# Kernel tuning notes

Hardware: AMD Instinct MI355X
Metric: run time of the kernel (lower is better)

## Reference

```python
import jax, jax.numpy as jnp
import numpy as np

V = 30      # vocab
D = 512     # hidden


def gru_cell(x, h, W_ih, W_hh, b_ih, b_hh):
    # PyTorch GRU cell math. x: [B, in], h: [B, D]
    gi = x @ W_ih.T + b_ih          # [B, 3D]
    gh = h @ W_hh.T + b_hh          # [B, 3D]
    i_r, i_z, i_n = jnp.split(gi, 3, axis=-1)
    h_r, h_z, h_n = jnp.split(gh, 3, axis=-1)
    r = jax.nn.sigmoid(i_r + h_r)
    z = jax.nn.sigmoid(i_z + h_z)
    n = jnp.tanh(i_n + r * h_n)
    return (1.0 - z) * n + z * h


def setup_inputs() -> dict:
    key = jax.random.key(0)
    ks = jax.random.split(key, 16)
    B, T, S = 64, 200, 1024
    p = 0.05  # param scale
    return {
        "initial_decoder_hidden": jax.random.normal(ks[0], (2, B, D), jnp.float32),
        "targets": jax.random.randint(ks[1], (B, T), 0, V),
        "encoder_outputs": jax.random.normal(ks[2], (B, S, D), jnp.float32),
        "W_ih0": jax.random.normal(ks[3], (3 * D, V), jnp.float32) * p,
        "W_hh0": jax.random.normal(ks[4], (3 * D, D), jnp.float32) * p,
        "b_ih0": jax.random.normal(ks[5], (3 * D,), jnp.float32) * p,
        "b_hh0": jax.random.normal(ks[6], (3 * D,), jnp.float32) * p,
        "W_ih1": jax.random.normal(ks[7], (3 * D, D), jnp.float32) * p,
        "W_hh1": jax.random.normal(ks[8], (3 * D, D), jnp.float32) * p,
        "b_ih1": jax.random.normal(ks[9], (3 * D,), jnp.float32) * p,
        "b_hh1": jax.random.normal(ks[10], (3 * D,), jnp.float32) * p,
        "W_out": jax.random.normal(ks[11], (D, 2 * D), jnp.float32) * p,
        "W_tok": jax.random.normal(ks[12], (V, D), jnp.float32) * p,
        "b_tok": jax.random.normal(ks[13], (V,), jnp.float32) * p,
    }


def reference(initial_decoder_hidden, targets, encoder_outputs,
              W_ih0, W_hh0, b_ih0, b_hh0,
              W_ih1, W_hh1, b_ih1, b_hh1,
              W_out, W_tok, b_tok):
    # Teacher-forced decode. Original feeds one_hot(targets[:,0]) at t=0,
    # then one_hot(targets[:,t]) AFTER step t, i.e. step t>0 consumes
    # one_hot(targets[:, t-1]).
    B, T = targets.shape
    idx = jnp.concatenate([targets[:, :1], targets[:, :-1]], axis=1)  # [B, T]
    xs = jax.nn.one_hot(idx, V, dtype=jnp.float32)                    # [B, T, V]
    xs = jnp.swapaxes(xs, 0, 1)                                       # [T, B, V]

    mem = encoder_outputs  # [B, S, D]

    def step(carry, x):
        h0, h1 = carry
        h0 = gru_cell(x, h0, W_ih0, W_hh0, b_ih0, b_hh0)
        h1 = gru_cell(h0, h1, W_ih1, W_hh1, b_ih1, b_hh1)
        q = h1                                              # [B, D] top-layer hidden
        scores = jnp.einsum("bd,bsd->bs", q, mem)           # dot attention
        a = jax.nn.softmax(scores, axis=-1)                 # [B, S]
        c = jnp.einsum("bs,bsd->bd", a, mem)                # context [B, D]
        attn_h = jnp.tanh(jnp.concatenate([c, q], axis=-1) @ W_out.T)  # [B, D]
        logits = attn_h @ W_tok.T + b_tok                   # [B, V]
        return (h0, h1), logits

    h_init = (initial_decoder_hidden[0], initial_decoder_hidden[1])
    _, logits = jax.lax.scan(step, h_init, xs)              # [T, B, V]
    return jnp.swapaxes(logits, 0, 1)                       # [B, T, V]
```

## Files before the change

kernel.cpp:

```cpp
#include <hip/hip_runtime.h>

#define TT 200
#define SS 1024
#define DD 512
#define VV 30
#define BB 64
#define BBDD (BB*DD)

#define WS_H0   0
#define WS_GI   (2*BBDD)
#define WS_H1A  (WS_GI + 2*1536*64)
#define WS_CALL (WS_H1A + 200*BBDD)

typedef __attribute__((ext_vector_type(4))) float f4;

__device__ __forceinline__ float dot4(f4 a, f4 b) {
  return a.x*b.x + a.y*b.y + a.z*b.z + a.w*b.w;
}
__device__ __forceinline__ float sigmoidf_(float x) { return 1.f/(1.f + __expf(-x)); }

__device__ __forceinline__ void gl_lds16(const void* g, void* l) {
  __builtin_amdgcn_global_load_lds(
      (const __attribute__((address_space(1))) unsigned int*)g,
      (__attribute__((address_space(3))) unsigned int*)l,
      16, 0, 0);
}

__device__ __forceinline__ void stage64(const float* src, float* TILE, int wv, int lane) {
  #pragma unroll
  for (int rr = 0; rr < 8; ++rr) {
    const int row = wv*8 + rr;
    const float* g = src + (size_t)row*DD + lane*4;
    gl_lds16(g,       TILE + row*516);
    gl_lds16(g + 256, TILE + row*516 + 256);
  }
}

__device__ __forceinline__ void wave_dots(const float* TILE, const float* W, const float* bias,
                                          float* GH, int w_id, int wv, int lane) {
  const int c0 = wv*3, c1 = c0+1, c2 = c0+2;
  const int R0 = __builtin_amdgcn_readfirstlane(((c0>>3)<<9) + w_id*8 + (c0&7));
  const int R1 = __builtin_amdgcn_readfirstlane(((c1>>3)<<9) + w_id*8 + (c1&7));
  const int R2 = __builtin_amdgcn_readfirstlane(((c2>>3)<<9) + w_id*8 + (c2&7));
  const f4* w0 = (const f4*)(W + (size_t)R0*DD);
  const f4* w1 = (const f4*)(W + (size_t)R1*DD);
  const f4* w2 = (const f4*)(W + (size_t)R2*DD);
  const f4* hv4 = (const f4*)TILE + (size_t)lane*129;
  float a0=0.f, a1=0.f, a2=0.f;
  #pragma unroll 4
  for (int kq = 0; kq < 128; ++kq) {
    f4 h = hv4[kq];
    a0 += dot4(h, w0[kq]); a1 += dot4(h, w1[kq]); a2 += dot4(h, w2[kq]);
  }
  GH[c0*64 + lane] = a0 + bias[R0];
  GH[c1*64 + lane] = a1 + bias[R1];
  GH[c2*64 + lane] = a2 + bias[R2];
}

__device__ __forceinline__ void wave_dots_g(const float* TILE, const float* W, const float* bias,
                                            float* gi, int w_id, int wv, int lane) {
  const int c0 = wv*3, c1 = c0+1, c2 = c0+2;
  const int R0 = __builtin_amdgcn_readfirstlane(((c0>>3)<<9) + w_id*8 + (c0&7));
  const int R1 = __builtin_amdgcn_readfirstlane(((c1>>3)<<9) + w_id*8 + (c1&7));
  const int R2 = __builtin_amdgcn_readfirstlane(((c2>>3)<<9) + w_id*8 + (c2&7));
  const f4* w0 = (const f4*)(W + (size_t)R0*DD);
  const f4* w1 = (const f4*)(W + (size_t)R1*DD);
  const f4* w2 = (const f4*)(W + (size_t)R2*DD);
  const f4* hv4 = (const f4*)TILE + (size_t)lane*129;
  float a0=0.f, a1=0.f, a2=0.f;
  #pragma unroll 4
  for (int kq = 0; kq < 128; ++kq) {
    f4 h = hv4[kq];
    a0 += dot4(h, w0[kq]); a1 += dot4(h, w1[kq]); a2 += dot4(h, w2[kq]);
  }
  gi[(size_t)R0*64 + lane] = a0 + bias[R0];
  gi[(size_t)R1*64 + lane] = a1 + bias[R1];
  gi[(size_t)R2*64 + lane] = a2 + bias[R2];
}

__launch_bounds__(512, 1)
__global__ void k_gru0(const float* __restrict__ h0prev, const int* __restrict__ targets,
                       const float* __restrict__ W_ih0, const float* __restrict__ W_hh0,
                       const float* __restrict__ b_ih0, const float* __restrict__ b_hh0,
                       float* __restrict__ h0out, int tokcol) {
  __shared__ float SM[34560];
  float* const TILE = SM;
  float* const GHX  = SM + 33024;
  const int tid = threadIdx.x, bid = blockIdx.x;
  const int lane = tid & 63, wv = tid >> 6;
  stage64(h0prev, TILE, wv, lane);
  __syncthreads();
  wave_dots(TILE, W_hh0, b_hh0, GHX, bid, wv, lane);
  __syncthreads();
  const int dl = tid >> 6, bb = tid & 63, d = bid*8 + dl;
  const int tok = targets[bb*TT + tokcol];
  float gir = W_ih0[(size_t)d*VV + tok]          + b_ih0[d];
  float giz = W_ih0[(size_t)(DD + d)*VV + tok]   + b_ih0[DD + d];
  float gin = W_ih0[(size_t)(2*DD + d)*VV + tok] + b_ih0[2*DD + d];
  float r_ = sigmoidf_(gir + GHX[(0*8 + dl)*64 + bb]);
  float z_ = sigmoidf_(giz + GHX[(1*8 + dl)*64 + bb]);
  float n_ = tanhf(gin + r_*GHX[(2*8 + dl)*64 + bb]);
  float h0old = TILE[bb*516 + d];
  h0out[(size_t)bb*DD + d] = (1.f - z_)*n_ + z_*h0old;
}

__launch_bounds__(512, 1)
__global__ void k_pro1(const float* __restrict__ h0buf0, const int* __restrict__ targets,
                       const float* __restrict__ W_ih0, const float* __restrict__ W_hh0,
                       const float* __restrict__ b_ih0, const float* __restrict__ b_hh0,
                       const float* __restrict__ W_ih1, const float* __restrict__ b_ih1,
                       float* __restrict__ h0buf1, float* __restrict__ gibuf0) {
  __shared__ float SM[34560];
  float* const TILE = SM;
  float* const GHX  = SM + 33024;
  const int tid = threadIdx.x, bid = blockIdx.x;
  const int lane = tid & 63, wv = tid >> 6;
  stage64(h0buf0, TILE, wv, lane);
  __syncthreads();
  if (bid < 64) {
    wave_dots(TILE, W_hh0, b_hh0, GHX, bid, wv, lane);
    __syncthreads();
    const int dl = tid >> 6, bb = tid & 63, d = bid*8 + dl;
    const int tok = targets[bb*TT + 0];
    float gir = W_ih0[(size_t)d*VV + tok]          + b_ih0[d];
    float giz = W_ih0[(size_t)(DD + d)*VV + tok]   + b_ih0[DD + d];
    float gin = W_ih0[(size_t)(2*DD + d)*VV + tok] + b_ih0[2*DD + d];
    float r_ = sigmoidf_(gir + GHX[(0*8 + dl)*64 + bb]);
    float z_ = sigmoidf_(giz + GHX[(1*8 + dl)*64 + bb]);
    float n_ = tanhf(gin + r_*GHX[(2*8 + dl)*64 + bb]);
    float h0old = TILE[bb*516 + d];
    h0buf1[(size_t)bb*DD + d] = (1.f - z_)*n_ + z_*h0old;
  } else {
    wave_dots_g(TILE, W_ih1, b_ih1, gibuf0, bid - 64, wv, lane);
  }
}

__launch_bounds__(512, 1)
__global__ void k_chain(const float* __restrict__ h0rd, float* __restrict__ h0wr,
                        const float* __restrict__ h1src, float* __restrict__ h1dst,
                        const float* __restrict__ gird, float* __restrict__ giwr,
                        const int* __restrict__ targets,
                        const float* __restrict__ W_ih0, const float* __restrict__ W_hh0,
                        const float* __restrict__ b_ih0, const float* __restrict__ b_hh0,
                        const float* __restrict__ W_hh1, const float* __restrict__ b_hh1,
                        const float* __restrict__ W_ih1, const float* __restrict__ b_ih1,
                        int t) {
  __shared__ float SM[34560];
  float* const TILE = SM;
  float* const GHX  = SM + 33024;
  const int tid = threadIdx.x, bid = blockIdx.x;
  const int lane = tid & 63, wv = tid >> 6;
  const int dl = tid >> 6, bb = tid & 63;

  if (bid < 64) {
    if (t <= 197) {
      const int d = bid*8 + dl;
      stage64(h0rd, TILE, wv, lane);
      __syncthreads();
      wave_dots(TILE, W_hh0, b_hh0, GHX, bid, wv, lane);
      __syncthreads();
      const int tok = targets[bb*TT + (t + 1)];
      float gir = W_ih0[(size_t)d*VV + tok]          + b_ih0[d];
      float giz = W_ih0[(size_t)(DD + d)*VV + tok]   + b_ih0[DD + d];
      float gin = W_ih0[(size_t)(2*DD + d)*VV + tok] + b_ih0[2*DD + d];
      float r_ = sigmoidf_(gir + GHX[(0*8 + dl)*64 + bb]);
      float z_ = sigmoidf_(giz + GHX[(1*8 + dl)*64 + bb]);
      float n_ = tanhf(gin + r_*GHX[(2*8 + dl)*64 + bb]);
      float h0old = TILE[bb*516 + d];
      h0wr[(size_t)bb*DD + d] = (1.f - z_)*n_ + z_*h0old;
    }
  } else if (bid < 128) {
    const int w_id = bid - 64;
    const int d = w_id*8 + dl;
    stage64(h1src, TILE, wv, lane);
    __syncthreads();
    wave_dots(TILE, W_hh1, b_hh1, GHX, w_id, wv, lane);
    float h1old = TILE[bb*516 + d];
    __syncthreads();
    float gir = gird[(size_t)(0*DD + d)*64 + bb];
    float giz = gird[(size_t)(1*DD + d)*64 + bb];
    float gin = gird[(size_t)(2*DD + d)*64 + bb];
    float r_ = sigmoidf_(gir + GHX[(0*8 + dl)*64 + bb]);
    float z_ = sigmoidf_(giz + GHX[(1*8 + dl)*64 + bb]);
    float n_ = tanhf(gin + r_*GHX[(2*8 + dl)*64 + bb]);
    h1dst[(size_t)bb*DD + d] = (1.f - z_)*n_ + z_*h1old;
  } else {
    if (t <= 198) {
      stage64(h0rd, TILE, wv, lane);
      __syncthreads();
      wave_dots_g(TILE, W_ih1, b_ih1, giwr, bid - 128, wv, lane);
    }
  }
}

__launch_bounds__(512, 1)
__global__ void k_attn_all(const float* __restrict__ h1a, const float* __restrict__ mem,
                           float* __restrict__ call) {
  __shared__ float SM[37792];
  float* const QL  = SM + 16512;
  float* const SCR = SM + 37152;
  const int tid = threadIdx.x, bid = blockIdx.x;
  const int lane = tid & 63, wv = tid >> 6;
  const int b = bid / 5, tt = bid % 5;
  const int g = lane >> 2, sub = lane & 3;

  #pragma unroll
  for (int rr = 0; rr < 5; ++rr) {
    const int row = wv*5 + rr;
    const float* src = h1a + ((size_t)(tt*40 + row)*BB + b)*DD + lane*4;
    gl_lds16(src,       QL + row*516);
    gl_lds16(src + 256, QL + row*516 + 256);
  }
  const float* msrc = mem + (size_t)b*SS*DD;
  #pragma unroll
  for (int rr = 0; rr < 2; ++rr) {
    const int row = wv*2 + rr;
    const float* gsp = msrc + (size_t)row*DD + lane*4;
    gl_lds16(gsp,       SM + row*516);
    gl_lds16(gsp + 256, SM + row*516 + 256);
  }
  __syncthreads();

  f4 aa[5], ab[5]; float m[5], l[5];
  #pragma unroll
  for (int r = 0; r < 5; ++r) { aa[r] = (f4)0.f; ab[r] = (f4)0.f; m[r] = -3e38f; l[r] = 0.f; }

  int buf = 0;
  for (int tl = 0; tl < 64; ++tl) {
    if (tl + 1 < 64) {
      float* nb = SM + (buf^1)*8256;
      #pragma unroll
      for (int rr = 0; rr < 2; ++rr) {
        const int row = wv*2 + rr;
        const float* gsp = msrc + (size_t)(tl+1)*16*DD + (size_t)row*DD + lane*4;
        gl_lds16(gsp,       nb + row*516);
        gl_lds16(gsp + 256, nb + row*516 + 256);
      }
    }
    const f4* mtf4 = (const f4*)(SM + buf*8256);
    const f4* qlf4 = (const f4*)QL;

    float p[5] = {0.f, 0.f, 0.f, 0.f, 0.f};
    #pragma unroll 4
    for (int k = 0; k < 32; ++k) {
      const int idx = sub*32 + ((k + sub) & 31);
      const f4 mv = mtf4[g*129 + idx];
      #pragma unroll
      for (int r = 0; r < 5; ++r)
        p[r] += dot4(mv, qlf4[(wv*5 + r)*129 + idx]);
    }
    #pragma unroll
    for (int r = 0; r < 5; ++r) {
      p[r] += __shfl_xor(p[r], 1);
      p[r] += __shfl_xor(p[r], 2);
    }
    if (sub == 0) {
      #pragma unroll
      for (int r = 0; r < 5; ++r) SCR[wv*80 + r*16 + g] = p[r];
    }

    #pragma unroll
    for (int r = 0; r < 5; ++r) {
      float mx = SCR[wv*80 + r*16];
      #pragma unroll
      for (int s = 1; s < 16; ++s) mx = fmaxf(mx, SCR[wv*80 + r*16 + s]);
      const float mnew = fmaxf(m[r], mx);
      const float esc = __expf(m[r] - mnew);
      aa[r] *= esc; ab[r] *= esc; l[r] *= esc;
      m[r] = mnew;
    }
    for (int s = 0; s < 16; ++s) {
      const f4 ma = mtf4[s*129 + lane];
      const f4 mb = mtf4[s*129 + lane + 64];
      #pragma unroll
      for (int r = 0; r < 5; ++r) {
        const float w = __expf(SCR[wv*80 + r*16 + s] - m[r]);
        aa[r] += w*ma; ab[r] += w*mb; l[r] += w;
      }
    }
    __syncthreads();
    buf ^= 1;
  }

  #pragma unroll
  for (int r = 0; r < 5; ++r) {
    const float inv = 1.f / l[r];
    float* dst = call + ((size_t)(tt*40 + wv*5 + r)*BB + b)*DD;
    *(f4*)(dst + lane*4)       = aa[r]*inv;
    *(f4*)(dst + lane*4 + 256) = ab[r]*inv;
  }
}

__launch_bounds__(512, 1)
__global__ void k_outproj(const float* __restrict__ call, const float* __restrict__ h1a,
                          const float* __restrict__ W_out, const float* __restrict__ W_tok,
                          const float* __restrict__ b_tok, float* __restrict__ out) {
  __shared__ float SM[4352 + 33024];
  float* const XR = SM;
  float* const AH = SM + 4352;
  const int tid = threadIdx.x, bid = blockIdx.x;
  const int lane = tid & 63, wv = tid >> 6;
  const int rowbase = bid * 64;

  float acc[8][8];
  #pragma unroll
  for (int r = 0; r < 8; ++r)
    #pragma unroll
    for (int j = 0; j < 8; ++j) acc[r][j] = 0.f;

  for (int kc = 0; kc < 16; ++kc) {
    __syncthreads();
    {
      const int row = tid >> 3;
      const int kp  = (tid & 7) * 8;
      const int k   = kc*64 + kp;
      const size_t grow = (size_t)(rowbase + row) * DD;
      const float* src = (k < DD) ? (call + grow + k) : (h1a + grow + (k - DD));
      f4 v0 = *(const f4*)src;
      f4 v1 = *(const f4*)(src + 4);
      *(f4*)&XR[row*68 + kp]     = v0;
      *(f4*)&XR[row*68 + kp + 4] = v1;
    }
    __syncthreads();
    for (int k4 = 0; k4 < 16; ++k4) {
      f4 w4[8];
      #pragma unroll
      for (int j = 0; j < 8; ++j)
        w4[j] = *(const f4*)&W_out[(size_t)(lane*8 + j)*(2*DD) + kc*64 + k4*4];
      #pragma unroll
      for (int r = 0; r < 8; ++r) {
        const f4 x4 = *(const f4*)&XR[(wv*8 + r)*68 + k4*4];
        #pragma unroll
        for (int j = 0; j < 8; ++j) acc[r][j] += dot4(x4, w4[j]);
      }
    }
  }
  #pragma unroll
  for (int r = 0; r < 8; ++r) {
    f4 t0, t1;
    t0.x = tanhf(acc[r][0]); t0.y = tanhf(acc[r][1]); t0.z = tanhf(acc[r][2]); t0.w = tanhf(acc[r][3]);
    t1.x = tanhf(acc[r][4]); t1.y = tanhf(acc[r][5]); t1.z = tanhf(acc[r][6]); t1.w = tanhf(acc[r][7]);
    *(f4*)&AH[(wv*8 + r)*516 + lane*8]     = t0;
    *(f4*)&AH[(wv*8 + r)*516 + lane*8 + 4] = t1;
  }
  __syncthreads();
  const int v = tid & 31;
  const int rq = tid >> 5;
  if (v < VV) {
    for (int it = 0; it < 4; ++it) {
      const int row = rq + it*16;
      float s = 0.f;
      const f4* ar = (const f4*)&AH[row*516];
      const f4* wt = (const f4*)&W_tok[(size_t)v*DD];
      #pragma unroll 4
      for (int k4 = 0; k4 < 128; ++k4) s += dot4(ar[k4], wt[k4]);
      const int gr = rowbase + row;
      const int t = gr >> 6, b = gr & 63;
      out[((size_t)b*TT + t)*VV + v] = s + b_tok[v];
    }
  }
}

extern "C" void kernel_launch(void* const* d_in, const int* in_sizes, int n_in,
                              void* d_out, int out_size, void* d_ws, size_t ws_size,
                              hipStream_t stream) {
  const float* h_init = (const float*)d_in[0];
  const int*   targets= (const int*)d_in[1];
  const float* mem    = (const float*)d_in[2];
  const float* W_ih0  = (const float*)d_in[3];
  const float* W_hh0  = (const float*)d_in[4];
  const float* b_ih0  = (const float*)d_in[5];
  const float* b_hh0  = (const float*)d_in[6];
  const float* W_ih1  = (const float*)d_in[7];
  const float* W_hh1  = (const float*)d_in[8];
  const float* b_ih1  = (const float*)d_in[9];
  const float* b_hh1  = (const float*)d_in[10];
  const float* W_out  = (const float*)d_in[11];
  const float* W_tok  = (const float*)d_in[12];
  const float* b_tok  = (const float*)d_in[13];
  float* out = (float*)d_out;
  float* ws  = (float*)d_ws;

  float* h0b  = ws + WS_H0;
  float* gib  = ws + WS_GI;
  float* h1a  = ws + WS_H1A;
  float* call = ws + WS_CALL;

  hipLaunchKernelGGL(k_gru0, dim3(64), dim3(512), 0, stream,
                     h_init, targets, W_ih0, W_hh0, b_ih0, b_hh0, h0b, 0);
  hipLaunchKernelGGL(k_pro1, dim3(128), dim3(512), 0, stream,
                     h0b, targets, W_ih0, W_hh0, b_ih0, b_hh0,
                     W_ih1, b_ih1, h0b + BBDD, gib);

  for (int t = 0; t < TT; ++t) {
    const float* h0rd = h0b + (size_t)((t + 1) & 1)*BBDD;
    float*       h0wr = h0b + (size_t)(t & 1)*BBDD;
    const float* h1src= (t == 0) ? (h_init + BBDD) : (h1a + (size_t)(t - 1)*BBDD);
    float*       h1dst= h1a + (size_t)t*BBDD;
    const float* gird = gib + (size_t)(t & 1)*(1536*64);
    float*       giwr = gib + (size_t)((t + 1) & 1)*(1536*64);
    hipLaunchKernelGGL(k_chain, dim3(192), dim3(512), 0, stream,
                       h0rd, h0wr, h1src, h1dst, gird, giwr, targets,
                       W_ih0, W_hh0, b_ih0, b_hh0, W_hh1, b_hh1, W_ih1, b_ih1, t);
  }

  hipLaunchKernelGGL(k_attn_all, dim3(320), dim3(512), 0, stream, h1a, mem, call);

  hipLaunchKernelGGL(k_outproj, dim3(200), dim3(512), 0, stream,
                     call, h1a, W_out, W_tok, b_tok, out);
}
```

Baseline: 4.650 ms.

## Spread chain blocks across XCDs and retile attention to more, smaller blocks

```diff
diff --git a/kernel.cpp b/kernel.cpp
--- a/kernel.cpp
+++ b/kernel.cpp
@@ -47,7 +47,7 @@
   const f4* w2 = (const f4*)(W + (size_t)R2*DD);
   const f4* hv4 = (const f4*)TILE + (size_t)lane*129;
   float a0=0.f, a1=0.f, a2=0.f;
-  #pragma unroll 4
+  #pragma unroll 8
   for (int kq = 0; kq < 128; ++kq) {
     f4 h = hv4[kq];
     a0 += dot4(h, w0[kq]); a1 += dot4(h, w1[kq]); a2 += dot4(h, w2[kq]);
@@ -68,7 +68,7 @@
   const f4* w2 = (const f4*)(W + (size_t)R2*DD);
   const f4* hv4 = (const f4*)TILE + (size_t)lane*129;
   float a0=0.f, a1=0.f, a2=0.f;
-  #pragma unroll 4
+  #pragma unroll 8
   for (int kq = 0; kq < 128; ++kq) {
     f4 h = hv4[kq];
     a0 += dot4(h, w0[kq]); a1 += dot4(h, w1[kq]); a2 += dot4(h, w2[kq]);
@@ -151,13 +151,15 @@
   const int tid = threadIdx.x, bid = blockIdx.x;
   const int lane = tid & 63, wv = tid >> 6;
   const int dl = tid >> 6, bb = tid & 63;
-
-  if (bid < 64) {
-    if (t <= 197) {
-      const int d = bid*8 + dl;
+  const int xcd = bid & 7, brow = bid >> 3;
+
+  if (xcd < 3) {
+    const int k = brow*3 + xcd;
+    if (k < 64 && t <= 197) {
+      const int d = k*8 + dl;
       stage64(h0rd, TILE, wv, lane);
       __syncthreads();
-      wave_dots(TILE, W_hh0, b_hh0, GHX, bid, wv, lane);
+      wave_dots(TILE, W_hh0, b_hh0, GHX, k, wv, lane);
       __syncthreads();
       const int tok = targets[bb*TT + (t + 1)];
       float gir = W_ih0[(size_t)d*VV + tok]          + b_ih0[d];
@@ -169,112 +171,105 @@
       float h0old = TILE[bb*516 + d];
       h0wr[(size_t)bb*DD + d] = (1.f - z_)*n_ + z_*h0old;
     }
-  } else if (bid < 128) {
-    const int w_id = bid - 64;
-    const int d = w_id*8 + dl;
-    stage64(h1src, TILE, wv, lane);
-    __syncthreads();
-    wave_dots(TILE, W_hh1, b_hh1, GHX, w_id, wv, lane);
-    float h1old = TILE[bb*516 + d];
-    __syncthreads();
-    float gir = gird[(size_t)(0*DD + d)*64 + bb];
-    float giz = gird[(size_t)(1*DD + d)*64 + bb];
-    float gin = gird[(size_t)(2*DD + d)*64 + bb];
-    float r_ = sigmoidf_(gir + GHX[(0*8 + dl)*64 + bb]);
-    float z_ = sigmoidf_(giz + GHX[(1*8 + dl)*64 + bb]);
-    float n_ = tanhf(gin + r_*GHX[(2*8 + dl)*64 + bb]);
-    h1dst[(size_t)bb*DD + d] = (1.f - z_)*n_ + z_*h1old;
+  } else if (xcd < 6) {
+    const int k = brow*3 + (xcd - 3);
+    if (k < 64) {
+      const int d = k*8 + dl;
+      stage64(h1src, TILE, wv, lane);
+      __syncthreads();
+      wave_dots(TILE, W_hh1, b_hh1, GHX, k, wv, lane);
+      float h1old = TILE[bb*516 + d];
+      __syncthreads();
+      float gir = gird[(size_t)(0*DD + d)*64 + bb];
+      float giz = gird[(size_t)(1*DD + d)*64 + bb];
+      float gin = gird[(size_t)(2*DD + d)*64 + bb];
+      float r_ = sigmoidf_(gir + GHX[(0*8 + dl)*64 + bb]);
+      float z_ = sigmoidf_(giz + GHX[(1*8 + dl)*64 + bb]);
+      float n_ = tanhf(gin + r_*GHX[(2*8 + dl)*64 + bb]);
+      h1dst[(size_t)bb*DD + d] = (1.f - z_)*n_ + z_*h1old;
+    }
   } else {
-    if (t <= 198) {
+    const int k = brow*2 + (xcd - 6);
+    if (k < 64 && t <= 198) {
       stage64(h0rd, TILE, wv, lane);
       __syncthreads();
-      wave_dots_g(TILE, W_ih1, b_ih1, giwr, bid - 128, wv, lane);
-    }
-  }
-}
-
-__launch_bounds__(512, 1)
+      wave_dots_g(TILE, W_ih1, b_ih1, giwr, k, wv, lane);
+    }
+  }
+}
+
+__launch_bounds__(640, 1)
 __global__ void k_attn_all(const float* __restrict__ h1a, const float* __restrict__ mem,
                            float* __restrict__ call) {
-  __shared__ float SM[37792];
-  float* const QL  = SM + 16512;
-  float* const SCR = SM + 37152;
+  __shared__ float SM[18736];
+  float* const QL  = SM + 8256;
+  float* const SCR = SM + 8256 + 10320;
   const int tid = threadIdx.x, bid = blockIdx.x;
   const int lane = tid & 63, wv = tid >> 6;
-  const int b = bid / 5, tt = bid % 5;
-  const int g = lane >> 2, sub = lane & 3;
-
-  #pragma unroll
-  for (int rr = 0; rr < 5; ++rr) {
-    const int row = wv*5 + rr;
-    const float* src = h1a + ((size_t)(tt*40 + row)*BB + b)*DD + lane*4;
+  const int b = bid & 63, tt = bid >> 6;
+  const int g = lane >> 3, sub = lane & 7;
+
+  #pragma unroll
+  for (int rr = 0; rr < 2; ++rr) {
+    const int row = wv*2 + rr;
+    const float* src = h1a + ((size_t)(tt*20 + row)*BB + b)*DD + lane*4;
     gl_lds16(src,       QL + row*516);
     gl_lds16(src + 256, QL + row*516 + 256);
   }
   const float* msrc = mem + (size_t)b*SS*DD;
-  #pragma unroll
-  for (int rr = 0; rr < 2; ++rr) {
-    const int row = wv*2 + rr;
+  if (tid < 512) {
+    const int row = tid >> 6;
     const float* gsp = msrc + (size_t)row*DD + lane*4;
     gl_lds16(gsp,       SM + row*516);
     gl_lds16(gsp + 256, SM + row*516 + 256);
   }
   __syncthreads();
 
-  f4 aa[5], ab[5]; float m[5], l[5];
-  #pragma unroll
-  for (int r = 0; r < 5; ++r) { aa[r] = (f4)0.f; ab[r] = (f4)0.f; m[r] = -3e38f; l[r] = 0.f; }
+  f4 aa[2], ab[2]; float m[2], l[2];
+  #pragma unroll
+  for (int r = 0; r < 2; ++r) { aa[r] = (f4)0.f; ab[r] = (f4)0.f; m[r] = -3e38f; l[r] = 0.f; }
 
   int buf = 0;
-  for (int tl = 0; tl < 64; ++tl) {
-    if (tl + 1 < 64) {
-      float* nb = SM + (buf^1)*8256;
+  for (int tl = 0; tl < 128; ++tl) {
+    if (tl + 1 < 128 && tid < 512) {
+      float* nb = SM + (buf^1)*4128;
+      const int row = tid >> 6;
+      const float* gsp = msrc + ((size_t)(tl+1)*8 + row)*DD + lane*4;
+      gl_lds16(gsp,       nb + row*516);
+      gl_lds16(gsp + 256, nb + row*516 + 256);
+    }
+    const f4* mtf4 = (const f4*)(SM + buf*4128);
+    const f4* qlf4 = (const f4*)QL;
+
+    float p0 = 0.f, p1 = 0.f;
+    #pragma unroll 4
+    for (int k = 0; k < 16; ++k) {
+      const int idx = sub*16 + ((k + sub) & 15);
+      const f4 mv = mtf4[g*129 + idx];
+      p0 += dot4(mv, qlf4[(wv*2 + 0)*129 + idx]);
+      p1 += dot4(mv, qlf4[(wv*2 + 1)*129 + idx]);
+    }
+    p0 += __shfl_xor(p0, 1); p0 += __shfl_xor(p0, 2); p0 += __shfl_xor(p0, 4);
+    p1 += __shfl_xor(p1, 1); p1 += __shfl_xor(p1, 2); p1 += __shfl_xor(p1, 4);
+    if (sub == 0) { SCR[wv*16 + g] = p0; SCR[wv*16 + 8 + g] = p1; }
+
+    #pragma unroll
+    for (int r = 0; r < 2; ++r) {
+      float mx = SCR[wv*16 + r*8];
       #pragma unroll
-      for (int rr = 0; rr < 2; ++rr) {
-        const int row = wv*2 + rr;
-        const float* gsp = msrc + (size_t)(tl+1)*16*DD + (size_t)row*DD + lane*4;
-        gl_lds16(gsp,       nb + row*516);
-        gl_lds16(gsp + 256, nb + row*516 + 256);
-      }
-    }
-    const f4* mtf4 = (const f4*)(SM + buf*8256);
-    const f4* qlf4 = (const f4*)QL;
-
-    float p[5] = {0.f, 0.f, 0.f, 0.f, 0.f};
-    #pragma unroll 4
-    for (int k = 0; k < 32; ++k) {
-      const int idx = sub*32 + ((k + sub) & 31);
-      const f4 mv = mtf4[g*129 + idx];
-      #pragma unroll
-      for (int r = 0; r < 5; ++r)
-        p[r] += dot4(mv, qlf4[(wv*5 + r)*129 + idx]);
-    }
-    #pragma unroll
-    for (int r = 0; r < 5; ++r) {
-      p[r] += __shfl_xor(p[r], 1);
-      p[r] += __shfl_xor(p[r], 2);
-    }
-    if (sub == 0) {
-      #pragma unroll
-      for (int r = 0; r < 5; ++r) SCR[wv*80 + r*16 + g] = p[r];
-    }
-
-    #pragma unroll
-    for (int r = 0; r < 5; ++r) {
-      float mx = SCR[wv*80 + r*16];
-      #pragma unroll
-      for (int s = 1; s < 16; ++s) mx = fmaxf(mx, SCR[wv*80 + r*16 + s]);
+      for (int s = 1; s < 8; ++s) mx = fmaxf(mx, SCR[wv*16 + r*8 + s]);
       const float mnew = fmaxf(m[r], mx);
       const float esc = __expf(m[r] - mnew);
       aa[r] *= esc; ab[r] *= esc; l[r] *= esc;
       m[r] = mnew;
     }
-    for (int s = 0; s < 16; ++s) {
+    #pragma unroll
+    for (int s = 0; s < 8; ++s) {
       const f4 ma = mtf4[s*129 + lane];
-      const f4 mb = mtf4[s*129 + lane + 64];
+      const f4 mb = mtf4[s*129 + 64 + lane];
       #pragma unroll
-      for (int r = 0; r < 5; ++r) {
-        const float w = __expf(SCR[wv*80 + r*16 + s] - m[r]);
+      for (int r = 0; r < 2; ++r) {
+        const float w = __expf(SCR[wv*16 + r*8 + s] - m[r]);
         aa[r] += w*ma; ab[r] += w*mb; l[r] += w;
       }
     }
@@ -283,9 +278,9 @@
   }
 
   #pragma unroll
-  for (int r = 0; r < 5; ++r) {
+  for (int r = 0; r < 2; ++r) {
     const float inv = 1.f / l[r];
-    float* dst = call + ((size_t)(tt*40 + wv*5 + r)*BB + b)*DD;
+    float* dst = call + ((size_t)(tt*20 + wv*2 + r)*BB + b)*DD;
     *(f4*)(dst + lane*4)       = aa[r]*inv;
     *(f4*)(dst + lane*4 + 256) = ab[r]*inv;
   }
@@ -399,12 +394,12 @@
     float*       h1dst= h1a + (size_t)t*BBDD;
     const float* gird = gib + (size_t)(t & 1)*(1536*64);
     float*       giwr = gib + (size_t)((t + 1) & 1)*(1536*64);
-    hipLaunchKernelGGL(k_chain, dim3(192), dim3(512), 0, stream,
+    hipLaunchKernelGGL(k_chain, dim3(256), dim3(512), 0, stream,
                        h0rd, h0wr, h1src, h1dst, gird, giwr, targets,
                        W_ih0, W_hh0, b_ih0, b_hh0, W_hh1, b_hh1, W_ih1, b_ih1, t);
   }
 
-  hipLaunchKernelGGL(k_attn_all, dim3(320), dim3(512), 0, stream, h1a, mem, call);
+  hipLaunchKernelGGL(k_attn_all, dim3(640), dim3(640), 0, stream, h1a, mem, call);
 
   hipLaunchKernelGGL(k_outproj, dim3(200), dim3(512), 0, stream,
                      call, h1a, W_out, W_tok, b_tok, out);
```

Result: slower. 5.329 ms (+14.6%).
